# Kernel tuning notes

Measured on AMD Instinct MI355X. Metric: run time of the kernel, lower is better.

Reference implementation:

```python
import jax, jax.numpy as jnp
import numpy as np

B, L, ENC, DEC, ATT = 256, 196, 2048, 512, 512


def setup_inputs() -> dict:
    key = jax.random.key(0)
    ks = jax.random.split(key, 10)
    s = lambda d: 1.0 / np.sqrt(d)
    return {
        "x": jax.random.normal(ks[0], (B, L, ENC), dtype=jnp.float32),
        "h": jax.random.normal(ks[1], (B, DEC), dtype=jnp.float32),
        "W_enc": jax.random.uniform(ks[2], (ENC, ATT), jnp.float32, -s(ENC), s(ENC)),
        "b_enc": jax.random.uniform(ks[3], (ATT,), jnp.float32, -s(ENC), s(ENC)),
        "W_dec": jax.random.uniform(ks[4], (DEC, ATT), jnp.float32, -s(DEC), s(DEC)),
        "b_dec": jax.random.uniform(ks[5], (ATT,), jnp.float32, -s(DEC), s(DEC)),
        "W_full": jax.random.uniform(ks[6], (ATT, 1), jnp.float32, -s(ATT), s(ATT)),
        "b_full": jax.random.uniform(ks[7], (1,), jnp.float32, -s(ATT), s(ATT)),
        "W_beta": jax.random.uniform(ks[8], (DEC, 1), jnp.float32, -s(DEC), s(DEC)),
        "b_beta": jax.random.uniform(ks[9], (1,), jnp.float32, -s(DEC), s(DEC)),
    }


def reference(x, h, W_enc, b_enc, W_dec, b_dec, W_full, b_full, W_beta, b_beta):
    # x: [B, L, ENC], h: [B, DEC]
    att1 = jnp.einsum("blc,ca->bla", x, W_enc) + b_enc          # [B, L, ATT]
    att2 = h @ W_dec + b_dec                                     # [B, ATT]
    att = (jax.nn.relu(att1 + att2[:, None, :]) @ W_full)[..., 0] + b_full  # [B, L]
    alpha = jax.nn.softmax(att, axis=-1)                         # [B, L]
    z = jnp.einsum("bl,blc->bc", alpha, x)                       # [B, ENC]
    gate_beta = jax.nn.sigmoid(h @ W_beta + b_beta)              # [B, 1]
    return gate_beta * z, alpha
```

## Files before the change

### kernel.cpp

```cpp
#include <hip/hip_runtime.h>
#include <hip/hip_bf16.h>
#include <cstdint>

#define B_   256
#define L_   196
#define ENC_ 2048
#define DEC_ 512
#define ATT_ 512
#define M_TOT (B_*L_)

typedef short short8 __attribute__((ext_vector_type(8)));
typedef float f32x16 __attribute__((ext_vector_type(16)));

__device__ __forceinline__ unsigned short f2bf(float f) {
    union { float f; unsigned u; } v; v.f = f;
    unsigned u = v.u;
    return (unsigned short)((u + 0x7FFFu + ((u >> 16) & 1u)) >> 16);
}

__device__ __forceinline__ void gl_lds16(const void* g, void* l) {
    __builtin_amdgcn_global_load_lds((const __attribute__((address_space(1))) unsigned int*)g,
                                     (__attribute__((address_space(3))) unsigned int*)l,
                                     16, 0, 0);
}

__global__ void k_transpose(const float* __restrict__ W, unsigned short* __restrict__ WT) {
    __shared__ float S[32*33];
    const int k0 = blockIdx.x * 32, n0 = blockIdx.y * 32;
    const int t  = threadIdx.x;
    const int c31 = t & 31, q = t >> 5;
#pragma unroll
    for (int i = 0; i < 4; ++i) {
        int kl = q + i*8;
        S[c31*33 + kl] = W[(size_t)(k0+kl)*ATT_ + n0 + c31];
    }
    __syncthreads();
#pragma unroll
    for (int i = 0; i < 4; ++i) {
        int nn = q + i*8;
        WT[(size_t)(n0+nn)*ENC_ + k0 + c31] = f2bf(S[nn*33 + c31]);
    }
}

__global__ void k_prep2(const float* __restrict__ h, const float* __restrict__ Wdec,
                        const float* __restrict__ bdec, const float* __restrict__ benc,
                        const float* __restrict__ Wbeta, const float* __restrict__ bbeta,
                        float* __restrict__ att2c, float* __restrict__ gate) {
    const int b = blockIdx.x, t = threadIdx.x;
    __shared__ float hs[DEC_];
    __shared__ float pr[4];
    hs[t]       = h[(size_t)b*DEC_ + t];
    hs[t + 256] = h[(size_t)b*DEC_ + t + 256];
    __syncthreads();
    float a0 = 0.f, a1 = 0.f;
    for (int k = 0; k < DEC_; ++k) {
        float hk = hs[k];
        a0 = fmaf(hk, Wdec[(size_t)k*ATT_ + t],       a0);
        a1 = fmaf(hk, Wdec[(size_t)k*ATT_ + t + 256], a1);
    }
    att2c[(size_t)b*ATT_ + t]       = a0 + bdec[t]       + benc[t];
    att2c[(size_t)b*ATT_ + t + 256] = a1 + bdec[t + 256] + benc[t + 256];
    float p = hs[t]*Wbeta[t] + hs[t+256]*Wbeta[t+256];
#pragma unroll
    for (int mask = 32; mask; mask >>= 1) p += __shfl_xor(p, mask, 64);
    if ((t & 63) == 0) pr[t >> 6] = p;
    __syncthreads();
    if (t == 0) gate[b] = 1.f / (1.f + __expf(-(pr[0]+pr[1]+pr[2]+pr[3] + bbeta[0])));
}

__global__ __launch_bounds__(512, 4) void k_gemm(
        const float* __restrict__ x, const unsigned short* __restrict__ WT,
        const float* __restrict__ att2c, const float* __restrict__ Wfull,
        float* __restrict__ att) {
    __shared__ unsigned short Abuf[64*32];
    __shared__ unsigned short Bbuf[512*32];
    __shared__ float att_ws[8][64];

    const int tid   = threadIdx.x;
    const int wave  = tid >> 6;
    const int lane  = tid & 63;
    const int lane31 = lane & 31;
    const int laneh  = lane >> 5;
    const int m0 = blockIdx.x * 64;

    f32x16 acc[2][2];
#pragma unroll
    for (int i = 0; i < 2; ++i)
#pragma unroll
        for (int j = 0; j < 2; ++j)
#pragma unroll
            for (int r = 0; r < 16; ++r) acc[i][j][r] = 0.f;

    const int ar   = tid >> 3;
    const int ak4  = tid & 7;
    const int akc  = ak4 >> 1;
    const int ahalf= ak4 & 1;
    const int achunk = ar*4 + (akc ^ ((ar >> 1) & 3));
    const float* xrow = x + (size_t)(m0 + ar)*ENC_ + ak4*4;
    unsigned short* adst = Abuf + achunk*8 + ahalf*4;

    for (int k0 = 0; k0 < ENC_; k0 += 32) {
#pragma unroll
        for (int i = 0; i < 4; ++i) {
            int c  = wave*256 + i*64 + lane;
            int n  = c >> 2;
            int kc = (c & 3) ^ ((n >> 1) & 3);
            gl_lds16(WT + (size_t)n*ENC_ + k0 + kc*8,
                     (void*)(Bbuf + (wave*256 + i*64)*8));
        }
        float4 xa = *(const float4*)(xrow + k0);
        ushort4 pk;
        pk.x = f2bf(xa.x); pk.y = f2bf(xa.y); pk.z = f2bf(xa.z); pk.w = f2bf(xa.w);
        *(ushort4*)adst = pk;
        __syncthreads();

#pragma unroll
        for (int ks = 0; ks < 2; ++ks) {
            short8 a[2], bfr[2];
#pragma unroll
            for (int mi = 0; mi < 2; ++mi) {
                int m = mi*32 + lane31;
                int chunk = m*4 + ((ks*2 + laneh) ^ ((m >> 1) & 3));
                a[mi] = *(const short8*)(Abuf + chunk*8);
            }
#pragma unroll
            for (int ni = 0; ni < 2; ++ni) {
                int n = wave*64 + ni*32 + lane31;
                int chunk = n*4 + ((ks*2 + laneh) ^ ((n >> 1) & 3));
                bfr[ni] = *(const short8*)(Bbuf + chunk*8);
            }
#pragma unroll
            for (int mi = 0; mi < 2; ++mi)
#pragma unroll
                for (int ni = 0; ni < 2; ++ni)
                    acc[mi][ni] = __builtin_amdgcn_mfma_f32_32x32x16_bf16(
                                      a[mi], bfr[ni], acc[mi][ni], 0, 0, 0);
        }
        __syncthreads();
    }

    float* epi = (float*)Bbuf;
    {
        const int b0i = m0 / L_;
        const int b1i = (m0 + 63) / L_;
        epi[tid]        = Wfull[tid];
        epi[512 + tid]  = att2c[(size_t)b0i*ATT_ + tid];
        epi[1024 + tid] = att2c[(size_t)b1i*ATT_ + tid];
    }
    __syncthreads();
    const int split = (m0 / L_ + 1) * L_;
    const int n0 = wave*64 + lane31;
#pragma unroll
    for (int mi = 0; mi < 2; ++mi) {
#pragma unroll
        for (int reg = 0; reg < 16; ++reg) {
            int mloc = mi*32 + (reg & 3) + 8*(reg >> 2) + 4*laneh;
            int off  = (m0 + mloc >= split) ? 1024 : 512;
            float v0 = acc[mi][0][reg] + epi[off + n0];
            float v1 = acc[mi][1][reg] + epi[off + n0 + 32];
            v0 = fmaxf(v0, 0.f) * epi[n0];
            v1 = fmaxf(v1, 0.f) * epi[n0 + 32];
            float s = v0 + v1;
#pragma unroll
            for (int mask = 16; mask; mask >>= 1) s += __shfl_xor(s, mask, 64);
            if (lane31 == 0) att_ws[wave][mloc] = s;
        }
    }
    __syncthreads();
    if (tid < 64) {
        float r = 0.f;
#pragma unroll
        for (int w = 0; w < 8; ++w) r += att_ws[w][tid];
        att[m0 + tid] = r;
    }
}

__global__ __launch_bounds__(512) void k_softz(
        const float* __restrict__ att, const float* __restrict__ x,
        const float* __restrict__ gate, float* __restrict__ out) {
    const int b = blockIdx.x, t = threadIdx.x;
    __shared__ float sa[L_];
    __shared__ float red[16];
    const int wid = t >> 6, lane = t & 63;
    float v = (t < L_) ? att[b*L_ + t] : -1e30f;
    float m = v;
#pragma unroll
    for (int mask = 32; mask; mask >>= 1) m = fmaxf(m, __shfl_xor(m, mask, 64));
    if (lane == 0) red[wid] = m;
    __syncthreads();
    m = red[0];
#pragma unroll
    for (int w = 1; w < 8; ++w) m = fmaxf(m, red[w]);
    float e = (t < L_) ? __expf(v - m) : 0.f;
    float s = e;
#pragma unroll
    for (int mask = 32; mask; mask >>= 1) s += __shfl_xor(s, mask, 64);
    if (lane == 0) red[8 + wid] = s;
    __syncthreads();
    s = 0.f;
#pragma unroll
    for (int w = 0; w < 8; ++w) s += red[8 + w];
    float alpha = e / s;
    if (t < L_) { sa[t] = alpha; out[(size_t)B_*ENC_ + (size_t)b*L_ + t] = alpha; }
    __syncthreads();
    const float* xb = x + (size_t)b*L_*ENC_ + t*4;
    float4 z = {0.f, 0.f, 0.f, 0.f};
#pragma unroll 4
    for (int l = 0; l < L_; ++l) {
        float a = sa[l];
        float4 u = *(const float4*)(xb + (size_t)l*ENC_);
        z.x += a*u.x; z.y += a*u.y; z.z += a*u.z; z.w += a*u.w;
    }
    const float g = gate[b];
    float4 o; o.x = g*z.x; o.y = g*z.y; o.z = g*z.z; o.w = g*z.w;
    *(float4*)(out + (size_t)b*ENC_ + t*4) = o;
}

extern "C" void kernel_launch(void* const* d_in, const int* in_sizes, int n_in,
                              void* d_out, int out_size, void* d_ws, size_t ws_size,
                              hipStream_t stream) {
    const float* x      = (const float*)d_in[0];
    const float* h      = (const float*)d_in[1];
    const float* W_enc  = (const float*)d_in[2];
    const float* b_enc  = (const float*)d_in[3];
    const float* W_dec  = (const float*)d_in[4];
    const float* b_dec  = (const float*)d_in[5];
    const float* W_full = (const float*)d_in[6];
    const float* W_beta = (const float*)d_in[8];
    const float* b_beta = (const float*)d_in[9];
    float* out = (float*)d_out;

    char* ws = (char*)d_ws;
    unsigned short* WT = (unsigned short*)ws;
    float* att2c  = (float*)(ws + 2*1024*1024);
    float* gate   = (float*)(ws + 2*1024*1024 + 512*1024);
    float* attbuf = (float*)(ws + 2*1024*1024 + 512*1024 + 1024);

    k_transpose<<<dim3(ENC_/32, ATT_/32), 256, 0, stream>>>(W_enc, WT);
    k_prep2   <<<B_, 256, 0, stream>>>(h, W_dec, b_dec, b_enc, W_beta, b_beta, att2c, gate);
    k_gemm    <<<M_TOT/64, 512, 0, stream>>>(x, WT, att2c, W_full, attbuf);
    k_softz   <<<B_, 512, 0, stream>>>(attbuf, x, gate, out);
}
```

Measured before the change: 815.0 us.

## Double-buffer GEMM LDS tiles with 4-wave blocks and split softmax-z over ENC

```diff
diff --git a/kernel.cpp b/kernel.cpp
--- a/kernel.cpp
+++ b/kernel.cpp
@@ -68,13 +68,13 @@
     if (t == 0) gate[b] = 1.f / (1.f + __expf(-(pr[0]+pr[1]+pr[2]+pr[3] + bbeta[0])));
 }
 
-__global__ __launch_bounds__(512, 4) void k_gemm(
+__global__ __launch_bounds__(256, 2) void k_gemm(
         const float* __restrict__ x, const unsigned short* __restrict__ WT,
         const float* __restrict__ att2c, const float* __restrict__ Wfull,
         float* __restrict__ att) {
-    __shared__ unsigned short Abuf[64*32];
-    __shared__ unsigned short Bbuf[512*32];
-    __shared__ float att_ws[8][64];
+    __shared__ alignas(16) unsigned short Ab[2][64*32];
+    __shared__ alignas(16) unsigned short Bb[2][512*32];
+    __shared__ float att_ws[4][64];
 
     const int tid   = threadIdx.x;
     const int wave  = tid >> 6;
@@ -83,104 +83,122 @@
     const int laneh  = lane >> 5;
     const int m0 = blockIdx.x * 64;
 
-    f32x16 acc[2][2];
+    f32x16 acc[2][4];
 #pragma unroll
     for (int i = 0; i < 2; ++i)
 #pragma unroll
-        for (int j = 0; j < 2; ++j)
+        for (int j = 0; j < 4; ++j)
 #pragma unroll
             for (int r = 0; r < 16; ++r) acc[i][j][r] = 0.f;
 
-    const int ar   = tid >> 3;
-    const int ak4  = tid & 7;
-    const int akc  = ak4 >> 1;
-    const int ahalf= ak4 & 1;
-    const int achunk = ar*4 + (akc ^ ((ar >> 1) & 3));
-    const float* xrow = x + (size_t)(m0 + ar)*ENC_ + ak4*4;
-    unsigned short* adst = Abuf + achunk*8 + ahalf*4;
+    int boff[8];
+#pragma unroll
+    for (int j = 0; j < 8; ++j) {
+        int c  = (wave*8 + j)*64 + lane;
+        int n  = c >> 2;
+        int kc = (c & 3) ^ ((n >> 1) & 3);
+        boff[j] = n*ENC_ + kc*8;
+    }
+    const int ar = tid >> 2, g = tid & 3;
+    const int achunk = ar*4 + (g ^ ((ar >> 1) & 3));
+    const float* xrow = x + (size_t)(m0 + ar)*ENC_ + g*8;
+
+#pragma unroll
+    for (int j = 0; j < 8; ++j)
+        gl_lds16(WT + boff[j], (void*)&Bb[0][(wave*8 + j)*512]);
+    float4 pa = *(const float4*)(xrow);
+    float4 pb = *(const float4*)(xrow + 4);
+    {
+        short8 w;
+        w[0] = f2bf(pa.x); w[1] = f2bf(pa.y); w[2] = f2bf(pa.z); w[3] = f2bf(pa.w);
+        w[4] = f2bf(pb.x); w[5] = f2bf(pb.y); w[6] = f2bf(pb.z); w[7] = f2bf(pb.w);
+        *(short8*)&Ab[0][achunk*8] = w;
+    }
 
     for (int k0 = 0; k0 < ENC_; k0 += 32) {
-#pragma unroll
-        for (int i = 0; i < 4; ++i) {
-            int c  = wave*256 + i*64 + lane;
-            int n  = c >> 2;
-            int kc = (c & 3) ^ ((n >> 1) & 3);
-            gl_lds16(WT + (size_t)n*ENC_ + k0 + kc*8,
-                     (void*)(Bbuf + (wave*256 + i*64)*8));
-        }
-        float4 xa = *(const float4*)(xrow + k0);
-        ushort4 pk;
-        pk.x = f2bf(xa.x); pk.y = f2bf(xa.y); pk.z = f2bf(xa.z); pk.w = f2bf(xa.w);
-        *(ushort4*)adst = pk;
+        const int cur = (k0 >> 5) & 1, nxt = cur ^ 1;
         __syncthreads();
-
+        const bool more = (k0 + 32) < ENC_;
+        if (more) {
+#pragma unroll
+            for (int j = 0; j < 8; ++j)
+                gl_lds16(WT + boff[j] + (k0 + 32), (void*)&Bb[nxt][(wave*8 + j)*512]);
+            pa = *(const float4*)(xrow + k0 + 32);
+            pb = *(const float4*)(xrow + k0 + 36);
+        }
 #pragma unroll
         for (int ks = 0; ks < 2; ++ks) {
-            short8 a[2], bfr[2];
+            short8 a[2], bf[4];
 #pragma unroll
             for (int mi = 0; mi < 2; ++mi) {
-                int m = mi*32 + lane31;
-                int chunk = m*4 + ((ks*2 + laneh) ^ ((m >> 1) & 3));
-                a[mi] = *(const short8*)(Abuf + chunk*8);
+                int m  = mi*32 + lane31;
+                int ch = m*4 + ((ks*2 + laneh) ^ ((m >> 1) & 3));
+                a[mi] = *(const short8*)&Ab[cur][ch*8];
             }
 #pragma unroll
-            for (int ni = 0; ni < 2; ++ni) {
-                int n = wave*64 + ni*32 + lane31;
-                int chunk = n*4 + ((ks*2 + laneh) ^ ((n >> 1) & 3));
-                bfr[ni] = *(const short8*)(Bbuf + chunk*8);
+            for (int ni = 0; ni < 4; ++ni) {
+                int n  = wave*128 + ni*32 + lane31;
+                int ch = n*4 + ((ks*2 + laneh) ^ ((n >> 1) & 3));
+                bf[ni] = *(const short8*)&Bb[cur][ch*8];
             }
 #pragma unroll
             for (int mi = 0; mi < 2; ++mi)
 #pragma unroll
-                for (int ni = 0; ni < 2; ++ni)
+                for (int ni = 0; ni < 4; ++ni)
                     acc[mi][ni] = __builtin_amdgcn_mfma_f32_32x32x16_bf16(
-                                      a[mi], bfr[ni], acc[mi][ni], 0, 0, 0);
-        }
-        __syncthreads();
-    }
-
-    float* epi = (float*)Bbuf;
+                                      a[mi], bf[ni], acc[mi][ni], 0, 0, 0);
+        }
+        if (more) {
+            short8 w;
+            w[0] = f2bf(pa.x); w[1] = f2bf(pa.y); w[2] = f2bf(pa.z); w[3] = f2bf(pa.w);
+            w[4] = f2bf(pb.x); w[5] = f2bf(pb.y); w[6] = f2bf(pb.z); w[7] = f2bf(pb.w);
+            *(short8*)&Ab[nxt][achunk*8] = w;
+        }
+    }
+
+    float* epi = (float*)&Bb[0][0];
     {
         const int b0i = m0 / L_;
         const int b1i = (m0 + 63) / L_;
         epi[tid]        = Wfull[tid];
+        epi[256 + tid]  = Wfull[256 + tid];
         epi[512 + tid]  = att2c[(size_t)b0i*ATT_ + tid];
+        epi[768 + tid]  = att2c[(size_t)b0i*ATT_ + 256 + tid];
         epi[1024 + tid] = att2c[(size_t)b1i*ATT_ + tid];
+        epi[1280 + tid] = att2c[(size_t)b1i*ATT_ + 256 + tid];
     }
     __syncthreads();
     const int split = (m0 / L_ + 1) * L_;
-    const int n0 = wave*64 + lane31;
 #pragma unroll
     for (int mi = 0; mi < 2; ++mi) {
 #pragma unroll
         for (int reg = 0; reg < 16; ++reg) {
-            int mloc = mi*32 + (reg & 3) + 8*(reg >> 2) + 4*laneh;
+            int r32  = (reg & 3) + 8*(reg >> 2) + 4*laneh;
+            int mloc = mi*32 + r32;
             int off  = (m0 + mloc >= split) ? 1024 : 512;
-            float v0 = acc[mi][0][reg] + epi[off + n0];
-            float v1 = acc[mi][1][reg] + epi[off + n0 + 32];
-            v0 = fmaxf(v0, 0.f) * epi[n0];
-            v1 = fmaxf(v1, 0.f) * epi[n0 + 32];
-            float s = v0 + v1;
-#pragma unroll
-            for (int mask = 16; mask; mask >>= 1) s += __shfl_xor(s, mask, 64);
-            if (lane31 == 0) att_ws[wave][mloc] = s;
-        }
-    }
-    __syncthreads();
-    if (tid < 64) {
-        float r = 0.f;
-#pragma unroll
-        for (int w = 0; w < 8; ++w) r += att_ws[w][tid];
-        att[m0 + tid] = r;
-    }
-}
-
-__global__ __launch_bounds__(512) void k_softz(
+            float v = 0.f;
+#pragma unroll
+            for (int ni = 0; ni < 4; ++ni) {
+                int n = wave*128 + ni*32 + lane31;
+                float tv = acc[mi][ni][reg] + epi[off + n];
+                v = fmaf(fmaxf(tv, 0.f), epi[n], v);
+            }
+#pragma unroll
+            for (int mask = 16; mask; mask >>= 1) v += __shfl_xor(v, mask, 64);
+            if (lane31 == 0) att_ws[wave][mloc] = v;
+        }
+    }
+    __syncthreads();
+    if (tid < 64)
+        att[m0 + tid] = att_ws[0][tid] + att_ws[1][tid] + att_ws[2][tid] + att_ws[3][tid];
+}
+
+__global__ __launch_bounds__(256) void k_softz(
         const float* __restrict__ att, const float* __restrict__ x,
         const float* __restrict__ gate, float* __restrict__ out) {
-    const int b = blockIdx.x, t = threadIdx.x;
+    const int b = blockIdx.x, s = blockIdx.y, t = threadIdx.x;
     __shared__ float sa[L_];
-    __shared__ float red[16];
+    __shared__ float red[8];
     const int wid = t >> 6, lane = t & 63;
     float v = (t < L_) ? att[b*L_ + t] : -1e30f;
     float m = v;
@@ -188,32 +206,32 @@
     for (int mask = 32; mask; mask >>= 1) m = fmaxf(m, __shfl_xor(m, mask, 64));
     if (lane == 0) red[wid] = m;
     __syncthreads();
-    m = red[0];
-#pragma unroll
-    for (int w = 1; w < 8; ++w) m = fmaxf(m, red[w]);
+    m = fmaxf(fmaxf(red[0], red[1]), fmaxf(red[2], red[3]));
     float e = (t < L_) ? __expf(v - m) : 0.f;
-    float s = e;
-#pragma unroll
-    for (int mask = 32; mask; mask >>= 1) s += __shfl_xor(s, mask, 64);
-    if (lane == 0) red[8 + wid] = s;
-    __syncthreads();
-    s = 0.f;
-#pragma unroll
-    for (int w = 0; w < 8; ++w) s += red[8 + w];
-    float alpha = e / s;
-    if (t < L_) { sa[t] = alpha; out[(size_t)B_*ENC_ + (size_t)b*L_ + t] = alpha; }
-    __syncthreads();
-    const float* xb = x + (size_t)b*L_*ENC_ + t*4;
+    float sum = e;
+#pragma unroll
+    for (int mask = 32; mask; mask >>= 1) sum += __shfl_xor(sum, mask, 64);
+    if (lane == 0) red[4 + wid] = sum;
+    __syncthreads();
+    sum = red[4] + red[5] + red[6] + red[7];
+    float alpha = e / sum;
+    if (t < L_) {
+        sa[t] = alpha;
+        if (s == 0) out[(size_t)B_*ENC_ + (size_t)b*L_ + t] = alpha;
+    }
+    __syncthreads();
+    const float* xb = x + (size_t)b*L_*ENC_ + s*1024 + t*4;
     float4 z = {0.f, 0.f, 0.f, 0.f};
-#pragma unroll 4
+#pragma unroll 7
     for (int l = 0; l < L_; ++l) {
         float a = sa[l];
         float4 u = *(const float4*)(xb + (size_t)l*ENC_);
-        z.x += a*u.x; z.y += a*u.y; z.z += a*u.z; z.w += a*u.w;
+        z.x = fmaf(a, u.x, z.x); z.y = fmaf(a, u.y, z.y);
+        z.z = fmaf(a, u.z, z.z); z.w = fmaf(a, u.w, z.w);
     }
     const float g = gate[b];
     float4 o; o.x = g*z.x; o.y = g*z.y; o.z = g*z.z; o.w = g*z.w;
-    *(float4*)(out + (size_t)b*ENC_ + t*4) = o;
+    *(float4*)(out + (size_t)b*ENC_ + s*1024 + t*4) = o;
 }
 
 extern "C" void kernel_launch(void* const* d_in, const int* in_sizes, int n_in,
@@ -238,6 +256,6 @@
 
     k_transpose<<<dim3(ENC_/32, ATT_/32), 256, 0, stream>>>(W_enc, WT);
     k_prep2   <<<B_, 256, 0, stream>>>(h, W_dec, b_dec, b_enc, W_beta, b_beta, att2c, gate);
-    k_gemm    <<<M_TOT/64, 512, 0, stream>>>(x, WT, att2c, W_full, attbuf);
-    k_softz   <<<B_, 512, 0, stream>>>(attbuf, x, gate, out);
-}
+    k_gemm    <<<M_TOT/64, 256, 0, stream>>>(x, WT, att2c, W_full, attbuf);
+    k_softz   <<<dim3(B_, 2), 256, 0, stream>>>(attbuf, x, gate, out);
+}
```

New measurement: 772.1 us. 5.3% less time.
